# Kernel optimization log

Hardware: AMD Instinct MI355X
Metric: run time of the kernel (lower is better)

The kernel has to match this reference:

```python
import jax, jax.numpy as jnp
import numpy as np

B, D, NN = 16, 2, 100        # batch, num_depots, num_nodes (pickups+deliveries)
N2 = NN // 2                 # pickups (= deliveries)
NA = D + NN                  # total nodes per batch graph
H, HE, L = 128, 64, 3        # hidden_node_dim, hidden_edge_dim, conv_layers
SLOPE, EPS = 0.2, 1e-5


def _bn(x, g, b):
    # BatchNorm1d in training mode: per-feature batch stats (biased var)
    m = jnp.mean(x, axis=0)
    v = jnp.var(x, axis=0)
    return (x - m) * jax.lax.rsqrt(v + EPS) * g + b


def _leaky(x):
    return jnp.where(x >= 0, x, SLOPE * x)


def _prop(xk, e, m, Wg):
    # Dense-equivalent of GatConv.propagate over a fully-connected per-batch grid.
    # Edge (i, j): x_i = x[target j], x_j = x[source i] (matches edge_index layout:
    # row0 = i repeated, row1 = j blockwise; PyG target = edge_index[1]).
    # xk: [B, N, H] transformed node feats; e: [B, N, N, HE]; m: [B, N, N] 0/1.
    h = xk.shape[-1]
    wi, wj, we = Wg[:h], Wg[h:2 * h], Wg[2 * h:]  # split cat([x_i, x_j, e]) @ Wg
    alpha = _leaky((xk @ wi)[:, None, :, :]        # x_i contribution (target j)
                   + (xk @ wj)[:, :, None, :]      # x_j contribution (source i)
                   + jnp.einsum('bijc,ch->bijh', e, we))
    alpha = jnp.where(m[..., None] != 0, alpha, -jnp.inf)
    alpha = jax.nn.softmax(alpha, axis=1)          # segment softmax keyed by target j
    return jnp.einsum('bijh,bih->bjh', alpha, xk)  # scatter-add x_j * alpha to targets


def _forward(x, demand, time_window, edge_attr_d, edge_attr_r,
             W0, W1, W2, W3, W4,
             b0_g, b0_b, b1_g, b1_b, b2_g, b2_b, b3_g, b3_b, b4_g, b4_b,
             ff_w1, ff_b1, ff_w2, ff_b2, bn_g, bn_b,
             Wvla, Wvlp, Wvld, Wga, Wgp, Wgd,
             edge_index, mask_adjacency_d, mask_adjacency_r):
    ds = jnp.concatenate([x, demand, time_window], axis=-1)  # [B, NA, 5]
    dep = _bn(ds[:, :D].reshape(B * D, -1) @ W0, b0_g, b0_b).reshape(B, D, H)
    pk_in = jnp.concatenate([ds[:, D:D + N2], ds[:, D + N2:D + NN]], axis=-1).reshape(B * N2, -1)
    pk = _bn(pk_in @ W1, b1_g, b1_b).reshape(B, N2, H)
    dl = _bn(ds[:, D + N2:D + NN].reshape(B * N2, -1) @ W2, b2_g, b2_b).reshape(B, N2, H)
    e_d = _bn(edge_attr_d.reshape(-1, edge_attr_d.shape[-1]) @ W3, b3_g, b3_b).reshape(B, NA, NA, HE)
    e_r = _bn(edge_attr_r.reshape(-1, edge_attr_r.shape[-1]) @ W4, b4_g, b4_b).reshape(B, NA, NA, HE)
    m_d = mask_adjacency_d.reshape(B, NA, NA)
    m_r = mask_adjacency_r.reshape(B, NA, NA)

    def conv(xc, e, m, l):
        xall = xc @ Wvla[l]
        pick = xc[:, D:D + N2] @ Wvlp[l]
        deli = xc[:, D + N2:D + NN] @ Wvld[l]
        X1 = _prop(xall, e, m, Wga[l])
        X2 = _prop(pick, e[:, D:D + N2, D:D + N2], m[:, D:D + N2, D:D + N2], Wgp[l])
        X3 = _prop(deli, e[:, D + N2:D + NN, D + N2:D + NN], m[:, D + N2:D + NN, D + N2:D + NN], Wgd[l])
        # faithful to torch.cat(dim=0) followed by view(B, -1, H)
        Xc = jnp.concatenate([X1.reshape(-1, H), X2.reshape(-1, H), X3.reshape(-1, H)], axis=0).reshape(B, -1, H)
        xa, xp, xdd = Xc[:, :NA], Xc[:, NA:NA + N2], Xc[:, NA + N2:NA + NN]
        return jnp.concatenate([xa[:, :D], xa[:, D:D + N2] + xp, xa[:, D + N2:] + xdd], axis=1)

    xd = jnp.concatenate([dep, pk, dl], axis=1)  # [B, NA, H]
    xr = xd
    for l in range(L):
        xd, xr = conv(xd, e_d, m_d, l), conv(xr, e_r, m_r, l)

    def ff_bn(xc):
        xf = xc.reshape(-1, H)
        f = jax.nn.relu(xf @ ff_w1 + ff_b1) @ ff_w2 + ff_b2
        return _bn(xf + f, bn_g, bn_b).reshape(B, NA, H)

    return ff_bn(xd), ff_bn(xr)


def setup_inputs() -> dict:
    key = jax.random.key(0)
    it = iter(jax.random.split(key, 40))

    def nrm(shape, s=0.05):
        return (s * jax.random.normal(next(it), shape)).astype(jnp.float32)

    def uni(shape):
        return jax.random.uniform(next(it), shape, dtype=jnp.float32)

    x = nrm((B, NA, 2), 1.0)
    # first D entries per batch are depots (demand == 0), rest are nonzero
    demand = jnp.concatenate([jnp.zeros((B, D, 1), jnp.float32), uni((B, NN, 1)) + 0.5], axis=1)
    time_window = uni((B, NA, 2))
    edge_attr_d = uni((B, NA * NA, 2))
    edge_attr_r = uni((B, NA * NA, 2))
    eye = jnp.eye(NA, dtype=jnp.int32)[None]
    mask_d = jnp.maximum(jax.random.randint(next(it), (B, NA, NA), 0, 2, dtype=jnp.int32), eye).reshape(B, NA * NA)
    mask_r = jnp.maximum(jax.random.randint(next(it), (B, NA, NA), 0, 2, dtype=jnp.int32), eye).reshape(B, NA * NA)
    ii = jnp.arange(B * NA, dtype=jnp.int32)
    edge_index = jnp.stack([jnp.repeat(ii, NA), jnp.repeat(ii.reshape(B, NA), NA, axis=0).reshape(-1)])

    inp = dict(
        x=x, demand=demand, time_window=time_window,
        edge_attr_d=edge_attr_d, edge_attr_r=edge_attr_r,
        W0=nrm((5, H)), W1=nrm((10, H)), W2=nrm((5, H)), W3=nrm((2, HE)), W4=nrm((2, HE)),
        b0_g=jnp.ones(H, jnp.float32), b0_b=jnp.zeros(H, jnp.float32),
        b1_g=jnp.ones(H, jnp.float32), b1_b=jnp.zeros(H, jnp.float32),
        b2_g=jnp.ones(H, jnp.float32), b2_b=jnp.zeros(H, jnp.float32),
        b3_g=jnp.ones(HE, jnp.float32), b3_b=jnp.zeros(HE, jnp.float32),
        b4_g=jnp.ones(HE, jnp.float32), b4_b=jnp.zeros(HE, jnp.float32),
        ff_w1=nrm((H, H)), ff_b1=jnp.zeros(H, jnp.float32),
        ff_w2=nrm((H, H)), ff_b2=jnp.zeros(H, jnp.float32),
        bn_g=jnp.ones(H, jnp.float32), bn_b=jnp.zeros(H, jnp.float32),
        Wvla=nrm((L, H, H)), Wvlp=nrm((L, H, H)), Wvld=nrm((L, H, H)),
        Wga=nrm((L, 2 * H + HE, H)), Wgp=nrm((L, 2 * H + HE, H)), Wgd=nrm((L, 2 * H + HE, H)),
        edge_index=edge_index, mask_adjacency_d=mask_d, mask_adjacency_r=mask_r,
    )
    return inp


def reference(x, demand, time_window, edge_attr_d, edge_attr_r,
              W0, W1, W2, W3, W4,
              b0_g, b0_b, b1_g, b1_b, b2_g, b2_b, b3_g, b3_b, b4_g, b4_b,
              ff_w1, ff_b1, ff_w2, ff_b2, bn_g, bn_b,
              Wvla, Wvlp, Wvld, Wga, Wgp, Wgd,
              edge_index, mask_adjacency_d, mask_adjacency_r):
    return _forward(x, demand, time_window, edge_attr_d, edge_attr_r,
                    W0, W1, W2, W3, W4,
                    b0_g, b0_b, b1_g, b1_b, b2_g, b2_b, b3_g, b3_b, b4_g, b4_b,
                    ff_w1, ff_b1, ff_w2, ff_b2, bn_g, bn_b,
                    Wvla, Wvlp, Wvld, Wga, Wgp, Wgd,
                    edge_index, mask_adjacency_d, mask_adjacency_r)
```

## Files before the change

### kernel.cpp

```cpp
#include <hip/hip_runtime.h>
#include <stdint.h>

#define B 16
#define D 2
#define NN 100
#define N2 50
#define NA 102
#define H 128
#define HE 64
#define L 3
#define SLOPE 0.2f
#define EPS 1e-5f

#define NAE (NA*NA)
#define EN (B*NAE)
#define R1 (B*NA)
#define R2 (B*N2)
#define RV (R1 + 2*R2)
#define NC 202
#define J 8
#define TI 34

#define ACC_MOM   0
#define ACC_NODE  16
#define ACC_FF    1024
#define OFF_PQR   2560
#define OFF_X0    9472
#define OFF_V     (OFF_X0 + R1*H)
#define OFF_AB    (OFF_V + 2*RV*H)
#define OFF_XO    (OFF_AB + 2*RV*2*H)
#define OFF_Z     (OFF_XO + 2*RV*H)

__device__ __forceinline__ void decode_vrow(int ridx, int& b, int& node) {
    if (ridx < R1) { b = ridx / NA; node = ridx % NA; }
    else if (ridx < R1 + R2) { int p = ridx - R1; b = p / N2; node = D + p % N2; }
    else { int p = ridx - R1 - R2; b = p / N2; node = D + N2 + p % N2; }
}
__device__ __forceinline__ void decode_nrow(int vr, int& b, int& node) {
    if (vr < 32) { b = vr >> 1; node = vr & 1; }
    else if (vr < 832) { int p = vr - 32; b = p / N2; node = D + p % N2; }
    else { int p = vr - 832; b = p / N2; node = D + N2 + p % N2; }
}
__device__ __forceinline__ float combined(const float* __restrict__ XO, int b, int node, int k) {
    float v = XO[(b*NC + node)*H + k];
    if (node >= D) v += XO[(b*NC + node + 100)*H + k];
    return v;
}

__global__ __launch_bounds__(256) void k_zero(float* __restrict__ ws) {
    for (int i = threadIdx.x; i < 2048; i += 256) ws[i] = 0.0f;
}

__global__ __launch_bounds__(256) void k_moments(const float* __restrict__ ea_d,
                                                 const float* __restrict__ ea_r,
                                                 float* __restrict__ ws) {
    int g = blockIdx.x >> 7;
    int bb = blockIdx.x & 127;
    const float2* ea = (const float2*)(g ? ea_r : ea_d);
    float s0 = 0, s1 = 0, s00 = 0, s11 = 0, s01 = 0;
    for (int idx = bb*256 + threadIdx.x; idx < EN; idx += 128*256) {
        float2 v = ea[idx];
        s0 += v.x; s1 += v.y; s00 += v.x*v.x; s11 += v.y*v.y; s01 += v.x*v.y;
    }
    __shared__ float sd[256];
    float vals[5] = {s0, s1, s00, s11, s01};
    for (int q = 0; q < 5; q++) {
        sd[threadIdx.x] = vals[q];
        __syncthreads();
        for (int off = 128; off > 0; off >>= 1) {
            if (threadIdx.x < off) sd[threadIdx.x] += sd[threadIdx.x + off];
            __syncthreads();
        }
        if (threadIdx.x == 0) atomicAdd(&ws[ACC_MOM + g*5 + q], sd[0]);
        __syncthreads();
    }
}

__global__ __launch_bounds__(128) void k_stpqr(const float* __restrict__ W3, const float* __restrict__ W4,
                                               const float* __restrict__ b3g, const float* __restrict__ b3b,
                                               const float* __restrict__ b4g, const float* __restrict__ b4b,
                                               const float* __restrict__ Wga, const float* __restrict__ Wgp,
                                               const float* __restrict__ Wgd, float* __restrict__ ws) {
    int bx = blockIdx.x;
    int g = bx / 9, rem = bx % 9, seg = rem / 3, l = rem % 3;
    __shared__ float st[192];
    int t = threadIdx.x;
    if (t < 64) {
        const float* W  = g ? W4 : W3;
        const float* gv = g ? b4g : b3g;
        const float* bv = g ? b4b : b3b;
        float Nr = (float)EN;
        float S0 = ws[ACC_MOM + g*5 + 0], S1 = ws[ACC_MOM + g*5 + 1];
        float S00 = ws[ACC_MOM + g*5 + 2], S11 = ws[ACC_MOM + g*5 + 3], S01 = ws[ACC_MOM + g*5 + 4];
        float w0 = W[t], w1 = W[64 + t];
        float m = (S0*w0 + S1*w1) / Nr;
        float E2 = (S00*w0*w0 + 2.0f*S01*w0*w1 + S11*w1*w1) / Nr;
        float var = E2 - m*m;
        float s = gv[t] * rsqrtf(var + EPS);
        st[t] = w0 * s; st[64 + t] = w1 * s; st[128 + t] = bv[t] - m*s;
    }
    __syncthreads();
    int h = t;
    const float* Wg = (seg == 0 ? Wga : (seg == 1 ? Wgp : Wgd)) + l*320*H;
    float P = 0, Q = 0, Rr = 0;
    for (int cc = 0; cc < HE; cc++) {
        float w = Wg[(2*H + cc)*H + h];
        P += st[cc]*w; Q += st[64 + cc]*w; Rr += st[128 + cc]*w;
    }
    float* o = ws + OFF_PQR + ((g*3 + seg)*3 + l)*384;
    o[h] = P; o[128 + h] = Q; o[256 + h] = Rr;
}

__global__ __launch_bounds__(128) void k_nodeinit(const float* __restrict__ x, const float* __restrict__ dm,
                                                  const float* __restrict__ tw,
                                                  const float* __restrict__ W0, const float* __restrict__ W1,
                                                  const float* __restrict__ W2, float* __restrict__ ws) {
    int c = threadIdx.x, bx = blockIdx.x;
    int seg = (bx < 2) ? 0 : (bx < 52 ? 1 : 2);
    const float* W = seg == 0 ? W0 : (seg == 1 ? W1 : W2);
    int nf = seg == 1 ? 10 : 5;
    float w[10];
    for (int f = 0; f < nf; f++) w[f] = W[f*H + c];
    float* x0 = ws + OFF_X0;
    float ls = 0, lss = 0;
    for (int r = 0; r < 16; r++) {
        int vr = bx*16 + r;
        int b, node; decode_nrow(vr, b, node);
        int row = b*NA + node;
        float y = x[row*2]*w[0] + x[row*2+1]*w[1] + dm[row]*w[2]
                + tw[row*2]*w[3] + tw[row*2+1]*w[4];
        if (seg == 1) {
            int r2 = row + N2;
            y += x[r2*2]*w[5] + x[r2*2+1]*w[6] + dm[r2]*w[7]
               + tw[r2*2]*w[8] + tw[r2*2+1]*w[9];
        }
        x0[row*H + c] = y;
        ls += y; lss += y*y;
    }
    atomicAdd(&ws[ACC_NODE + seg*256 + c], ls);
    atomicAdd(&ws[ACC_NODE + seg*256 + 128 + c], lss);
}

__global__ __launch_bounds__(128) void k_nodenorm(const float* __restrict__ b0g, const float* __restrict__ b0b,
                                                  const float* __restrict__ b1g, const float* __restrict__ b1b,
                                                  const float* __restrict__ b2g, const float* __restrict__ b2b,
                                                  float* __restrict__ ws) {
    int c = threadIdx.x, bx = blockIdx.x;
    int seg = (bx < 2) ? 0 : (bx < 52 ? 1 : 2);
    float cnt = seg == 0 ? 32.0f : 800.0f;
    float m = ws[ACC_NODE + seg*256 + c] / cnt;
    float v = ws[ACC_NODE + seg*256 + 128 + c] / cnt - m*m;
    const float* gp = seg == 0 ? b0g : (seg == 1 ? b1g : b2g);
    const float* bp = seg == 0 ? b0b : (seg == 1 ? b1b : b2b);
    float sc = gp[c] * rsqrtf(v + EPS);
    float sh = bp[c] - m*sc;
    float* x0 = ws + OFF_X0;
    for (int r = 0; r < 16; r++) {
        int vr = bx*16 + r;
        int b, node; decode_nrow(vr, b, node);
        int row = b*NA + node;
        x0[row*H + c] = x0[row*H + c]*sc + sh;
    }
}

__global__ __launch_bounds__(256) void k_gemmVA(const float* __restrict__ Wvla, const float* __restrict__ Wvlp,
                                                const float* __restrict__ Wvld,
                                                const float* __restrict__ Wga, const float* __restrict__ Wgp,
                                                const float* __restrict__ Wgd,
                                                int layer, float* __restrict__ ws) {
    __shared__ float xs[16][H];
    __shared__ float vs[16][H];
    int g = blockIdx.x / 202, tb = blockIdx.x % 202;
    int rowbase = tb * 16;
    const float* x0 = ws + OFF_X0;
    const float* XO = ws + OFF_XO + g*RV*H;
    for (int e = 0; e < 8; e++) {
        int lin = threadIdx.x + e*256;
        int r = lin >> 7, k = lin & 127;
        int b, node; decode_vrow(rowbase + r, b, node);
        xs[r][k] = (layer == 0) ? x0[(b*NA + node)*H + k] : combined(XO, b, node, k);
    }
    __syncthreads();
    int seg = rowbase < R1 ? 0 : (rowbase < R1 + R2 ? 1 : 2);
    const float* W = (seg == 0 ? Wvla : (seg == 1 ? Wvlp : Wvld)) + layer*H*H;
    int col = threadIdx.x & 127, half = threadIdx.x >> 7;
    float acc[8] = {0,0,0,0,0,0,0,0};
    const float* Wp = W + col;
    for (int k4 = 0; k4 < 32; k4++) {
        float w0 = Wp[(4*k4+0)*H], w1 = Wp[(4*k4+1)*H], w2 = Wp[(4*k4+2)*H], w3 = Wp[(4*k4+3)*H];
        #pragma unroll
        for (int rr = 0; rr < 8; rr++) {
            float4 x4 = *(const float4*)&xs[half + rr*2][4*k4];
            acc[rr] = fmaf(x4.w, w3, fmaf(x4.z, w2, fmaf(x4.y, w1, fmaf(x4.x, w0, acc[rr]))));
        }
    }
    float* V = ws + OFF_V + g*RV*H;
    #pragma unroll
    for (int rr = 0; rr < 8; rr++) {
        vs[half + rr*2][col] = acc[rr];
        V[(rowbase + half + rr*2)*H + col] = acc[rr];
    }
    __syncthreads();
    const float* Wg = (seg == 0 ? Wga : (seg == 1 ? Wgp : Wgd)) + layer*320*H;
    int c = threadIdx.x;
    const float* wb = Wg + ((c >> 7) * H) * H + (c & 127);
    float a2[16];
    #pragma unroll
    for (int rr = 0; rr < 16; rr++) a2[rr] = 0.0f;
    for (int k4 = 0; k4 < 32; k4++) {
        float w0 = wb[(4*k4+0)*H], w1 = wb[(4*k4+1)*H], w2 = wb[(4*k4+2)*H], w3 = wb[(4*k4+3)*H];
        #pragma unroll
        for (int rr = 0; rr < 16; rr++) {
            float4 v4 = *(const float4*)&vs[rr][4*k4];
            a2[rr] = fmaf(v4.w, w3, fmaf(v4.z, w2, fmaf(v4.y, w1, fmaf(v4.x, w0, a2[rr]))));
        }
    }
    float* AB = ws + OFF_AB + g*RV*2*H;
    #pragma unroll
    for (int rr = 0; rr < 16; rr++) AB[(rowbase + rr)*256 + c] = a2[rr];
}

__global__ __launch_bounds__(256) void k_attn(const float* __restrict__ ea_d, const float* __restrict__ ea_r,
                                              const int* __restrict__ mask_d, const int* __restrict__ mask_r,
                                              int layer, float* __restrict__ ws) {
    int k = blockIdx.x, y = blockIdx.y;
    int ci = y / 27, r = y % 27;
    int combo = k + 8*ci;
    int g = combo >> 4, b = combo & 15;
    int seg, jg, n, o, base;
    if (r < 13)      { seg = 0; jg = r;      n = NA; o = 0;      base = 0; }
    else if (r < 20) { seg = 1; jg = r - 13; n = N2; o = D;      base = R1; }
    else             { seg = 2; jg = r - 20; n = N2; o = D + N2; base = R1 + R2; }
    int j0 = jg * J;
    int jc = min(J, n - j0);
    int tid = threadIdx.x;
    int c = tid & 63, quad = tid >> 6;
    int jj0 = 2*quad, jj1 = 2*quad + 1;

    const float* pqr = ws + OFF_PQR + ((g*3 + seg)*3 + layer)*384;
    float2 Pv = ((const float2*)pqr)[c];
    float2 Qv = ((const float2*)(pqr + 128))[c];
    float2 Rv = ((const float2*)(pqr + 256))[c];
    const float2* ea = (const float2*)(g ? ea_r : ea_d);
    const int* mask = g ? mask_r : mask_d;
    const float* V  = ws + OFF_V  + g*RV*H   + base*H;
    const float* AB = ws + OFF_AB + g*RV*2*H + base*2*H;

    __shared__ float2 Bs[TI][64];
    __shared__ float2 Vs[TI][64];
    __shared__ float2 se[J][104];
    __shared__ int    msk_s[104];

    if (tid < n) {
        int ibase = b*NAE + (o + tid)*NA + o + j0;
        int bits = 0;
        #pragma unroll
        for (int jj = 0; jj < J; jj++) {
            int valid = (jj < jc) ? (mask[ibase + jj] != 0) : 0;
            bits |= valid << jj;
            se[jj][tid] = valid ? ea[ibase + jj] : make_float2(0.f, 0.f);
        }
        msk_s[tid] = bits;
    }

    float2 Aj0 = make_float2(0.f, 0.f), Aj1 = make_float2(0.f, 0.f);
    if (jj0 < jc) Aj0 = *(const float2*)&AB[(b*n + j0 + jj0)*256 + 2*c];
    if (jj1 < jc) Aj1 = *(const float2*)&AB[(b*n + j0 + jj1)*256 + 2*c];
    float A0x = Aj0.x + Rv.x, A0y = Aj0.y + Rv.y;
    float A1x = Aj1.x + Rv.x, A1y = Aj1.y + Rv.y;
    float2 l0 = make_float2(0.f, 0.f), a0 = make_float2(0.f, 0.f);
    float2 l1 = make_float2(0.f, 0.f), a1 = make_float2(0.f, 0.f);

    for (int t0 = 0; t0 < n; t0 += TI) {
        int rows = min(TI, n - t0);
        __syncthreads();
        for (int idx = tid; idx < rows*64; idx += 256) {
            int ir = idx >> 6, cc = idx & 63;
            int gi = b*n + t0 + ir;
            Bs[ir][cc] = *(const float2*)&AB[gi*256 + 128 + 2*cc];
            Vs[ir][cc] = *(const float2*)&V[gi*128 + 2*cc];
        }
        __syncthreads();
        for (int ir = 0; ir < rows; ir++) {
            int i = t0 + ir;
            int bits = msk_s[i];
            if (!(bits & ((1<<jj0) | (1<<jj1)))) continue;
            float2 Bi = Bs[ir][c];
            float2 Vi = Vs[ir][c];
            if (bits & (1<<jj0)) {
                float2 ev = se[jj0][i];
                float tx = fmaf(ev.x, Pv.x, fmaf(ev.y, Qv.x, A0x + Bi.x));
                float ty = fmaf(ev.x, Pv.y, fmaf(ev.y, Qv.y, A0y + Bi.y));
                tx = fminf(fmaxf(tx, SLOPE*tx), 80.0f);
                ty = fminf(fmaxf(ty, SLOPE*ty), 80.0f);
                float px = __expf(tx), py = __expf(ty);
                l0.x += px; l0.y += py;
                a0.x = fmaf(px, Vi.x, a0.x); a0.y = fmaf(py, Vi.y, a0.y);
            }
            if (bits & (1<<jj1)) {
                float2 ev = se[jj1][i];
                float tx = fmaf(ev.x, Pv.x, fmaf(ev.y, Qv.x, A1x + Bi.x));
                float ty = fmaf(ev.x, Pv.y, fmaf(ev.y, Qv.y, A1y + Bi.y));
                tx = fminf(fmaxf(tx, SLOPE*tx), 80.0f);
                ty = fminf(fmaxf(ty, SLOPE*ty), 80.0f);
                float px = __expf(tx), py = __expf(ty);
                l1.x += px; l1.y += py;
                a1.x = fmaf(px, Vi.x, a1.x); a1.y = fmaf(py, Vi.y, a1.y);
            }
        }
    }
    float* XO = ws + OFF_XO + g*RV*H + base*H;
    if (jj0 < jc)
        ((float2*)&XO[(b*n + j0 + jj0)*H])[c] = make_float2(a0.x/l0.x, a0.y/l0.y);
    if (jj1 < jc)
        ((float2*)&XO[(b*n + j0 + jj1)*H])[c] = make_float2(a1.x/l1.x, a1.y/l1.y);
}

__global__ __launch_bounds__(256) void k_ff(const float* __restrict__ ffw1, const float* __restrict__ ffb1,
                                            const float* __restrict__ ffw2, const float* __restrict__ ffb2,
                                            float* __restrict__ ws) {
    __shared__ float xs[16][H];
    __shared__ float hs[16][H];
    int g = blockIdx.x / 102, tb = blockIdx.x % 102;
    int rowbase = tb * 16;
    const float* XO = ws + OFF_XO + g*RV*H;
    for (int e = 0; e < 8; e++) {
        int lin = threadIdx.x + e*256;
        int r = lin >> 7, k = lin & 127;
        int ridx = rowbase + r;
        int b = ridx / NA, node = ridx % NA;
        xs[r][k] = combined(XO, b, node, k);
    }
    __syncthreads();
    int col = threadIdx.x & 127, half = threadIdx.x >> 7;
    float acc[8] = {0,0,0,0,0,0,0,0};
    const float* W1p = ffw1 + col;
    for (int k4 = 0; k4 < 32; k4++) {
        float w0 = W1p[(4*k4+0)*H], w1 = W1p[(4*k4+1)*H], w2 = W1p[(4*k4+2)*H], w3 = W1p[(4*k4+3)*H];
        #pragma unroll
        for (int rr = 0; rr < 8; rr++) {
            float4 x4 = *(const float4*)&xs[half + rr*2][4*k4];
            acc[rr] = fmaf(x4.w, w3, fmaf(x4.z, w2, fmaf(x4.y, w1, fmaf(x4.x, w0, acc[rr]))));
        }
    }
    float b1 = ffb1[col];
    #pragma unroll
    for (int rr = 0; rr < 8; rr++) {
        float hv = acc[rr] + b1;
        hs[half + rr*2][col] = hv > 0.0f ? hv : 0.0f;
    }
    __syncthreads();
    #pragma unroll
    for (int rr = 0; rr < 8; rr++) acc[rr] = 0.0f;
    const float* W2p = ffw2 + col;
    for (int k4 = 0; k4 < 32; k4++) {
        float w0 = W2p[(4*k4+0)*H], w1 = W2p[(4*k4+1)*H], w2 = W2p[(4*k4+2)*H], w3 = W2p[(4*k4+3)*H];
        #pragma unroll
        for (int rr = 0; rr < 8; rr++) {
            float4 x4 = *(const float4*)&hs[half + rr*2][4*k4];
            acc[rr] = fmaf(x4.w, w3, fmaf(x4.z, w2, fmaf(x4.y, w1, fmaf(x4.x, w0, acc[rr]))));
        }
    }
    float b2 = ffb2[col];
    float* Z = ws + OFF_Z + g*R1*H;
    float ls = 0, lss = 0;
    #pragma unroll
    for (int rr = 0; rr < 8; rr++) {
        int row = rowbase + half + rr*2;
        float z = acc[rr] + b2 + xs[half + rr*2][col];
        Z[row*H + col] = z;
        ls += z; lss += z*z;
    }
    atomicAdd(&ws[ACC_FF + g*256 + col], ls);
    atomicAdd(&ws[ACC_FF + g*256 + 128 + col], lss);
}

__global__ __launch_bounds__(256) void k_f3(const float* __restrict__ bng, const float* __restrict__ bnb,
                                            float* __restrict__ ws, float* __restrict__ out) {
    int eidx = blockIdx.x * 256 + threadIdx.x;
    int g = eidx / (R1*H);
    int c = eidx & 127;
    float m = ws[ACC_FF + g*256 + c] / 1632.0f;
    float v = ws[ACC_FF + g*256 + 128 + c] / 1632.0f - m*m;
    float sc = bng[c] * rsqrtf(v + EPS);
    float sh = bnb[c] - m*sc;
    out[eidx] = ws[OFF_Z + eidx] * sc + sh;
}

extern "C" void kernel_launch(void* const* d_in, const int* in_sizes, int n_in,
                              void* d_out, int out_size, void* d_ws, size_t ws_size,
                              hipStream_t stream) {
    const float* x    = (const float*)d_in[0];
    const float* dm   = (const float*)d_in[1];
    const float* tw   = (const float*)d_in[2];
    const float* ead  = (const float*)d_in[3];
    const float* ear  = (const float*)d_in[4];
    const float* W0   = (const float*)d_in[5];
    const float* W1   = (const float*)d_in[6];
    const float* W2   = (const float*)d_in[7];
    const float* W3   = (const float*)d_in[8];
    const float* W4   = (const float*)d_in[9];
    const float* b0g  = (const float*)d_in[10];
    const float* b0b  = (const float*)d_in[11];
    const float* b1g  = (const float*)d_in[12];
    const float* b1b  = (const float*)d_in[13];
    const float* b2g  = (const float*)d_in[14];
    const float* b2b  = (const float*)d_in[15];
    const float* b3g  = (const float*)d_in[16];
    const float* b3b  = (const float*)d_in[17];
    const float* b4g  = (const float*)d_in[18];
    const float* b4b  = (const float*)d_in[19];
    const float* ffw1 = (const float*)d_in[20];
    const float* ffb1 = (const float*)d_in[21];
    const float* ffw2 = (const float*)d_in[22];
    const float* ffb2 = (const float*)d_in[23];
    const float* bng  = (const float*)d_in[24];
    const float* bnb  = (const float*)d_in[25];
    const float* Wvla = (const float*)d_in[26];
    const float* Wvlp = (const float*)d_in[27];
    const float* Wvld = (const float*)d_in[28];
    const float* Wga  = (const float*)d_in[29];
    const float* Wgp  = (const float*)d_in[30];
    const float* Wgd  = (const float*)d_in[31];
    const int* mask_d = (const int*)d_in[33];
    const int* mask_r = (const int*)d_in[34];
    float* ws = (float*)d_ws;
    float* out = (float*)d_out;

    k_zero    <<<1, 256, 0, stream>>>(ws);
    k_moments <<<256, 256, 0, stream>>>(ead, ear, ws);
    k_stpqr   <<<18, 128, 0, stream>>>(W3, W4, b3g, b3b, b4g, b4b, Wga, Wgp, Wgd, ws);
    k_nodeinit<<<102, 128, 0, stream>>>(x, dm, tw, W0, W1, W2, ws);
    k_nodenorm<<<102, 128, 0, stream>>>(b0g, b0b, b1g, b1b, b2g, b2b, ws);
    for (int l = 0; l < L; l++) {
        k_gemmVA<<<404, 256, 0, stream>>>(Wvla, Wvlp, Wvld, Wga, Wgp, Wgd, l, ws);
        k_attn  <<<dim3(8, 108), 256, 0, stream>>>(ead, ear, mask_d, mask_r, l, ws);
    }
    k_ff<<<204, 256, 0, stream>>>(ffw1, ffb1, ffw2, ffb2, ws);
    k_f3<<<1632, 256, 0, stream>>>(bng, bnb, ws, out);
}
```

Measured before the change: 367.7 us.

## Split attention source range across two wave halves, halve GEMM row tiles, drop zero kernel

The attention kernel now runs 512 threads, with two halves each covering half of the source rows. Their partial sums are merged through shared memory before the final divide. The gemmVA and feed-forward kernels use 8-row tiles, which doubles the block count, and they software-prefetch the next weight quad. The zero-init kernel is removed: moments are written as per-block partials that k_stpqr reduces, and k_stpqr also zeroes the node accumulators. The aim is more parallelism, better occupancy and one less launch, at the cost of a merge step and less weight reuse per block.

```diff
diff --git a/kernel.cpp b/kernel.cpp
--- a/kernel.cpp
+++ b/kernel.cpp
@@ -21,11 +21,11 @@
 #define J 8
 #define TI 34
 
-#define ACC_MOM   0
-#define ACC_NODE  16
-#define ACC_FF    1024
-#define OFF_PQR   2560
-#define OFF_X0    9472
+#define MOM_PART  0
+#define ACC_NODE  1408
+#define ACC_FF    2176
+#define OFF_PQR   2816
+#define OFF_X0    9728
 #define OFF_V     (OFF_X0 + R1*H)
 #define OFF_AB    (OFF_V + 2*RV*H)
 #define OFF_XO    (OFF_AB + 2*RV*2*H)
@@ -45,10 +45,6 @@
     float v = XO[(b*NC + node)*H + k];
     if (node >= D) v += XO[(b*NC + node + 100)*H + k];
     return v;
-}
-
-__global__ __launch_bounds__(256) void k_zero(float* __restrict__ ws) {
-    for (int i = threadIdx.x; i < 2048; i += 256) ws[i] = 0.0f;
 }
 
 __global__ __launch_bounds__(256) void k_moments(const float* __restrict__ ea_d,
@@ -71,7 +67,7 @@
             if (threadIdx.x < off) sd[threadIdx.x] += sd[threadIdx.x + off];
             __syncthreads();
         }
-        if (threadIdx.x == 0) atomicAdd(&ws[ACC_MOM + g*5 + q], sd[0]);
+        if (threadIdx.x == 0) ws[MOM_PART + (g*128 + bb)*5 + q] = sd[0];
         __syncthreads();
     }
 }
@@ -83,15 +79,24 @@
                                                const float* __restrict__ Wgd, float* __restrict__ ws) {
     int bx = blockIdx.x;
     int g = bx / 9, rem = bx % 9, seg = rem / 3, l = rem % 3;
+    int t = threadIdx.x;
+    if (bx == 0) {
+        for (int i = t; i < 1280; i += 128) ws[ACC_NODE + i] = 0.0f;
+    }
+    __shared__ float momsh[5];
     __shared__ float st[192];
-    int t = threadIdx.x;
+    if (t < 5) {
+        float s = 0;
+        for (int p = 0; p < 128; p++) s += ws[MOM_PART + (g*128 + p)*5 + t];
+        momsh[t] = s;
+    }
+    __syncthreads();
     if (t < 64) {
         const float* W  = g ? W4 : W3;
         const float* gv = g ? b4g : b3g;
         const float* bv = g ? b4b : b3b;
         float Nr = (float)EN;
-        float S0 = ws[ACC_MOM + g*5 + 0], S1 = ws[ACC_MOM + g*5 + 1];
-        float S00 = ws[ACC_MOM + g*5 + 2], S11 = ws[ACC_MOM + g*5 + 3], S01 = ws[ACC_MOM + g*5 + 4];
+        float S0 = momsh[0], S1 = momsh[1], S00 = momsh[2], S11 = momsh[3], S01 = momsh[4];
         float w0 = W[t], w1 = W[64 + t];
         float m = (S0*w0 + S1*w1) / Nr;
         float E2 = (S00*w0*w0 + 2.0f*S01*w0*w1 + S11*w1*w1) / Nr;
@@ -168,35 +173,39 @@
                                                 const float* __restrict__ Wga, const float* __restrict__ Wgp,
                                                 const float* __restrict__ Wgd,
                                                 int layer, float* __restrict__ ws) {
-    __shared__ float xs[16][H];
-    __shared__ float vs[16][H];
-    int g = blockIdx.x / 202, tb = blockIdx.x % 202;
-    int rowbase = tb * 16;
+    __shared__ float xs[8][H];
+    __shared__ float vs[8][H];
+    int g = blockIdx.x / 404, tb = blockIdx.x % 404;
+    int rowbase = tb * 8;
     const float* x0 = ws + OFF_X0;
     const float* XO = ws + OFF_XO + g*RV*H;
-    for (int e = 0; e < 8; e++) {
+    for (int e = 0; e < 4; e++) {
         int lin = threadIdx.x + e*256;
         int r = lin >> 7, k = lin & 127;
         int b, node; decode_vrow(rowbase + r, b, node);
         xs[r][k] = (layer == 0) ? x0[(b*NA + node)*H + k] : combined(XO, b, node, k);
     }
     __syncthreads();
-    int seg = rowbase < R1 ? 0 : (rowbase < R1 + R2 ? 1 : 2);
+    int seg = tb < 204 ? 0 : (tb < 304 ? 1 : 2);
     const float* W = (seg == 0 ? Wvla : (seg == 1 ? Wvlp : Wvld)) + layer*H*H;
     int col = threadIdx.x & 127, half = threadIdx.x >> 7;
-    float acc[8] = {0,0,0,0,0,0,0,0};
+    float acc[4] = {0,0,0,0};
     const float* Wp = W + col;
+    float w0 = Wp[0], w1 = Wp[H], w2 = Wp[2*H], w3 = Wp[3*H];
     for (int k4 = 0; k4 < 32; k4++) {
-        float w0 = Wp[(4*k4+0)*H], w1 = Wp[(4*k4+1)*H], w2 = Wp[(4*k4+2)*H], w3 = Wp[(4*k4+3)*H];
+        int kn = ((k4 + 1) & 31) * 4;
+        const float* q = Wp + kn*H;
+        float n0 = q[0], n1 = q[H], n2 = q[2*H], n3 = q[3*H];
         #pragma unroll
-        for (int rr = 0; rr < 8; rr++) {
+        for (int rr = 0; rr < 4; rr++) {
             float4 x4 = *(const float4*)&xs[half + rr*2][4*k4];
             acc[rr] = fmaf(x4.w, w3, fmaf(x4.z, w2, fmaf(x4.y, w1, fmaf(x4.x, w0, acc[rr]))));
         }
+        w0 = n0; w1 = n1; w2 = n2; w3 = n3;
     }
     float* V = ws + OFF_V + g*RV*H;
     #pragma unroll
-    for (int rr = 0; rr < 8; rr++) {
+    for (int rr = 0; rr < 4; rr++) {
         vs[half + rr*2][col] = acc[rr];
         V[(rowbase + half + rr*2)*H + col] = acc[rr];
     }
@@ -204,23 +213,27 @@
     const float* Wg = (seg == 0 ? Wga : (seg == 1 ? Wgp : Wgd)) + layer*320*H;
     int c = threadIdx.x;
     const float* wb = Wg + ((c >> 7) * H) * H + (c & 127);
-    float a2[16];
-    #pragma unroll
-    for (int rr = 0; rr < 16; rr++) a2[rr] = 0.0f;
+    float a2[8];
+    #pragma unroll
+    for (int rr = 0; rr < 8; rr++) a2[rr] = 0.0f;
+    float v0 = wb[0], v1 = wb[H], v2 = wb[2*H], v3 = wb[3*H];
     for (int k4 = 0; k4 < 32; k4++) {
-        float w0 = wb[(4*k4+0)*H], w1 = wb[(4*k4+1)*H], w2 = wb[(4*k4+2)*H], w3 = wb[(4*k4+3)*H];
+        int kn = ((k4 + 1) & 31) * 4;
+        const float* q = wb + kn*H;
+        float n0 = q[0], n1 = q[H], n2 = q[2*H], n3 = q[3*H];
         #pragma unroll
-        for (int rr = 0; rr < 16; rr++) {
-            float4 v4 = *(const float4*)&vs[rr][4*k4];
-            a2[rr] = fmaf(v4.w, w3, fmaf(v4.z, w2, fmaf(v4.y, w1, fmaf(v4.x, w0, a2[rr]))));
-        }
+        for (int rr = 0; rr < 8; rr++) {
+            float4 x4 = *(const float4*)&vs[rr][4*k4];
+            a2[rr] = fmaf(x4.w, v3, fmaf(x4.z, v2, fmaf(x4.y, v1, fmaf(x4.x, v0, a2[rr]))));
+        }
+        v0 = n0; v1 = n1; v2 = n2; v3 = n3;
     }
     float* AB = ws + OFF_AB + g*RV*2*H;
     #pragma unroll
-    for (int rr = 0; rr < 16; rr++) AB[(rowbase + rr)*256 + c] = a2[rr];
-}
-
-__global__ __launch_bounds__(256) void k_attn(const float* __restrict__ ea_d, const float* __restrict__ ea_r,
+    for (int rr = 0; rr < 8; rr++) AB[(rowbase + rr)*256 + c] = a2[rr];
+}
+
+__global__ __launch_bounds__(512) void k_attn(const float* __restrict__ ea_d, const float* __restrict__ ea_r,
                                               const int* __restrict__ mask_d, const int* __restrict__ mask_r,
                                               int layer, float* __restrict__ ws) {
     int k = blockIdx.x, y = blockIdx.y;
@@ -234,8 +247,9 @@
     int j0 = jg * J;
     int jc = min(J, n - j0);
     int tid = threadIdx.x;
-    int c = tid & 63, quad = tid >> 6;
-    int jj0 = 2*quad, jj1 = 2*quad + 1;
+    int c = tid & 63, wv = tid >> 6;
+    int pair = wv & 3, ihalf = wv >> 2;
+    int jj0 = 2*pair, jj1 = 2*pair + 1;
 
     const float* pqr = ws + OFF_PQR + ((g*3 + seg)*3 + layer)*384;
     float2 Pv = ((const float2*)pqr)[c];
@@ -271,17 +285,23 @@
     float2 l0 = make_float2(0.f, 0.f), a0 = make_float2(0.f, 0.f);
     float2 l1 = make_float2(0.f, 0.f), a1 = make_float2(0.f, 0.f);
 
+    int nh = (n + 1) >> 1;
+    int i0w = ihalf ? nh : 0;
+    int i1w = ihalf ? n : nh;
+
     for (int t0 = 0; t0 < n; t0 += TI) {
         int rows = min(TI, n - t0);
         __syncthreads();
-        for (int idx = tid; idx < rows*64; idx += 256) {
+        for (int idx = tid; idx < rows*64; idx += 512) {
             int ir = idx >> 6, cc = idx & 63;
             int gi = b*n + t0 + ir;
             Bs[ir][cc] = *(const float2*)&AB[gi*256 + 128 + 2*cc];
             Vs[ir][cc] = *(const float2*)&V[gi*128 + 2*cc];
         }
         __syncthreads();
-        for (int ir = 0; ir < rows; ir++) {
+        int irlo = max(0, i0w - t0);
+        int irhi = min(rows, i1w - t0);
+        for (int ir = irlo; ir < irhi; ir++) {
             int i = t0 + ir;
             int bits = msk_s[i];
             if (!(bits & ((1<<jj0) | (1<<jj1)))) continue;
@@ -309,22 +329,37 @@
             }
         }
     }
-    float* XO = ws + OFF_XO + g*RV*H + base*H;
-    if (jj0 < jc)
-        ((float2*)&XO[(b*n + j0 + jj0)*H])[c] = make_float2(a0.x/l0.x, a0.y/l0.y);
-    if (jj1 < jc)
-        ((float2*)&XO[(b*n + j0 + jj1)*H])[c] = make_float2(a1.x/l1.x, a1.y/l1.y);
+    __syncthreads();
+    float* mg = (float*)Bs;
+    if (ihalf == 1) {
+        mg[(0*4 + pair)*64 + c] = l0.x;  mg[(1*4 + pair)*64 + c] = l0.y;
+        mg[(2*4 + pair)*64 + c] = l1.x;  mg[(3*4 + pair)*64 + c] = l1.y;
+        mg[(4*4 + pair)*64 + c] = a0.x;  mg[(5*4 + pair)*64 + c] = a0.y;
+        mg[(6*4 + pair)*64 + c] = a1.x;  mg[(7*4 + pair)*64 + c] = a1.y;
+    }
+    __syncthreads();
+    if (ihalf == 0) {
+        l0.x += mg[(0*4 + pair)*64 + c];  l0.y += mg[(1*4 + pair)*64 + c];
+        l1.x += mg[(2*4 + pair)*64 + c];  l1.y += mg[(3*4 + pair)*64 + c];
+        a0.x += mg[(4*4 + pair)*64 + c];  a0.y += mg[(5*4 + pair)*64 + c];
+        a1.x += mg[(6*4 + pair)*64 + c];  a1.y += mg[(7*4 + pair)*64 + c];
+        float* XO = ws + OFF_XO + g*RV*H + base*H;
+        if (jj0 < jc)
+            ((float2*)&XO[(b*n + j0 + jj0)*H])[c] = make_float2(a0.x/l0.x, a0.y/l0.y);
+        if (jj1 < jc)
+            ((float2*)&XO[(b*n + j0 + jj1)*H])[c] = make_float2(a1.x/l1.x, a1.y/l1.y);
+    }
 }
 
 __global__ __launch_bounds__(256) void k_ff(const float* __restrict__ ffw1, const float* __restrict__ ffb1,
                                             const float* __restrict__ ffw2, const float* __restrict__ ffb2,
                                             float* __restrict__ ws) {
-    __shared__ float xs[16][H];
-    __shared__ float hs[16][H];
-    int g = blockIdx.x / 102, tb = blockIdx.x % 102;
-    int rowbase = tb * 16;
+    __shared__ float xs[8][H];
+    __shared__ float hs[8][H];
+    int g = blockIdx.x / 204, tb = blockIdx.x % 204;
+    int rowbase = tb * 8;
     const float* XO = ws + OFF_XO + g*RV*H;
-    for (int e = 0; e < 8; e++) {
+    for (int e = 0; e < 4; e++) {
         int lin = threadIdx.x + e*256;
         int r = lin >> 7, k = lin & 127;
         int ridx = rowbase + r;
@@ -333,39 +368,47 @@
     }
     __syncthreads();
     int col = threadIdx.x & 127, half = threadIdx.x >> 7;
-    float acc[8] = {0,0,0,0,0,0,0,0};
+    float acc[4] = {0,0,0,0};
     const float* W1p = ffw1 + col;
+    float w0 = W1p[0], w1 = W1p[H], w2 = W1p[2*H], w3 = W1p[3*H];
     for (int k4 = 0; k4 < 32; k4++) {
-        float w0 = W1p[(4*k4+0)*H], w1 = W1p[(4*k4+1)*H], w2 = W1p[(4*k4+2)*H], w3 = W1p[(4*k4+3)*H];
+        int kn = ((k4 + 1) & 31) * 4;
+        const float* q = W1p + kn*H;
+        float n0 = q[0], n1 = q[H], n2 = q[2*H], n3 = q[3*H];
         #pragma unroll
-        for (int rr = 0; rr < 8; rr++) {
+        for (int rr = 0; rr < 4; rr++) {
             float4 x4 = *(const float4*)&xs[half + rr*2][4*k4];
             acc[rr] = fmaf(x4.w, w3, fmaf(x4.z, w2, fmaf(x4.y, w1, fmaf(x4.x, w0, acc[rr]))));
         }
+        w0 = n0; w1 = n1; w2 = n2; w3 = n3;
     }
     float b1 = ffb1[col];
     #pragma unroll
-    for (int rr = 0; rr < 8; rr++) {
+    for (int rr = 0; rr < 4; rr++) {
         float hv = acc[rr] + b1;
         hs[half + rr*2][col] = hv > 0.0f ? hv : 0.0f;
     }
     __syncthreads();
     #pragma unroll
-    for (int rr = 0; rr < 8; rr++) acc[rr] = 0.0f;
+    for (int rr = 0; rr < 4; rr++) acc[rr] = 0.0f;
     const float* W2p = ffw2 + col;
+    w0 = W2p[0]; w1 = W2p[H]; w2 = W2p[2*H]; w3 = W2p[3*H];
     for (int k4 = 0; k4 < 32; k4++) {
-        float w0 = W2p[(4*k4+0)*H], w1 = W2p[(4*k4+1)*H], w2 = W2p[(4*k4+2)*H], w3 = W2p[(4*k4+3)*H];
+        int kn = ((k4 + 1) & 31) * 4;
+        const float* q = W2p + kn*H;
+        float n0 = q[0], n1 = q[H], n2 = q[2*H], n3 = q[3*H];
         #pragma unroll
-        for (int rr = 0; rr < 8; rr++) {
+        for (int rr = 0; rr < 4; rr++) {
             float4 x4 = *(const float4*)&hs[half + rr*2][4*k4];
             acc[rr] = fmaf(x4.w, w3, fmaf(x4.z, w2, fmaf(x4.y, w1, fmaf(x4.x, w0, acc[rr]))));
         }
+        w0 = n0; w1 = n1; w2 = n2; w3 = n3;
     }
     float b2 = ffb2[col];
     float* Z = ws + OFF_Z + g*R1*H;
     float ls = 0, lss = 0;
     #pragma unroll
-    for (int rr = 0; rr < 8; rr++) {
+    for (int rr = 0; rr < 4; rr++) {
         int row = rowbase + half + rr*2;
         float z = acc[rr] + b2 + xs[half + rr*2][col];
         Z[row*H + col] = z;
@@ -427,15 +470,14 @@
     float* ws = (float*)d_ws;
     float* out = (float*)d_out;
 
-    k_zero    <<<1, 256, 0, stream>>>(ws);
     k_moments <<<256, 256, 0, stream>>>(ead, ear, ws);
     k_stpqr   <<<18, 128, 0, stream>>>(W3, W4, b3g, b3b, b4g, b4b, Wga, Wgp, Wgd, ws);
     k_nodeinit<<<102, 128, 0, stream>>>(x, dm, tw, W0, W1, W2, ws);
     k_nodenorm<<<102, 128, 0, stream>>>(b0g, b0b, b1g, b1b, b2g, b2b, ws);
     for (int l = 0; l < L; l++) {
-        k_gemmVA<<<404, 256, 0, stream>>>(Wvla, Wvlp, Wvld, Wga, Wgp, Wgd, l, ws);
-        k_attn  <<<dim3(8, 108), 256, 0, stream>>>(ead, ear, mask_d, mask_r, l, ws);
-    }
-    k_ff<<<204, 256, 0, stream>>>(ffw1, ffb1, ffw2, ffb2, ws);
+        k_gemmVA<<<808, 256, 0, stream>>>(Wvla, Wvlp, Wvld, Wga, Wgp, Wgd, l, ws);
+        k_attn  <<<dim3(8, 108), 512, 0, stream>>>(ead, ear, mask_d, mask_r, l, ws);
+    }
+    k_ff<<<408, 256, 0, stream>>>(ffw1, ffb1, ffw2, ffb2, ws);
     k_f3<<<1632, 256, 0, stream>>>(bng, bnb, ws, out);
 }
```

Result: faster. 327.4 us (-10.9%).
